# Optimization experiments

Measured on AMD Instinct MI355X. Metric: run time of the kernel, lower is better.

## Reference

```python
import jax, jax.numpy as jnp
import numpy as np

TIMESTEPS = 32
MAX_LATENCY = 1.0


def setup_inputs() -> dict:
    key = jax.random.key(0)
    data = jax.random.uniform(key, (32, 256, 256), dtype=jnp.float32)
    return {"data": data}


def reference(data):
    # data: [B, H, W] (any trailing dims). Output: [B, T, H, W].
    T = TIMESTEPS
    d_min = data.min()
    d_max = data.max()
    denom = jnp.maximum(d_max - d_min, jnp.asarray(1e-12, data.dtype))
    normalized = jnp.where(d_max > d_min, (data - d_min) / denom,
                           jnp.full_like(data, 0.5))
    latencies = (1.0 - normalized) * MAX_LATENCY
    # torch .long() truncates toward zero; latencies >= 0 so floor == trunc
    spike_times = jnp.clip((latencies * (T - 1)).astype(jnp.int32), 0, T - 1)
    # one-hot over timestep axis, then move it next to batch: [B, ..., T] -> [B, T, ...]
    spike_train = jax.nn.one_hot(spike_times, T, dtype=jnp.float32)
    return jnp.moveaxis(spike_train, -1, 1)
```

## Files before the change

kernel.cpp:

```cpp
#include <hip/hip_runtime.h>

#define TSTEPS 32
#define HW 65536
#define NB 32
#define N_ELEM (NB * HW)
#define N4 (N_ELEM / 4)
#define RED_BLOCKS 1024

__device__ __forceinline__ unsigned int f2key(float f) {
    unsigned int u = __float_as_uint(f);
    return (u & 0x80000000u) ? ~u : (u | 0x80000000u);
}
__device__ __forceinline__ float key2f(unsigned int k) {
    unsigned int u = (k & 0x80000000u) ? (k & 0x7fffffffu) : ~k;
    return __uint_as_float(u);
}

__global__ void lc_partial(const float4* __restrict__ in, unsigned int* __restrict__ ws) {
    __shared__ unsigned int smin[4], sinv[4];
    int tid = threadIdx.x;
    int i0  = blockIdx.x * 512 + tid;
    unsigned int kmin = 0xFFFFFFFFu, kinv = 0xFFFFFFFFu;
    #pragma unroll
    for (int j = 0; j < 2; ++j) {
        float4 v = in[i0 + j * 256];
        unsigned int k;
        k = f2key(v.x); kmin = min(kmin, k); kinv = min(kinv, ~k);
        k = f2key(v.y); kmin = min(kmin, k); kinv = min(kinv, ~k);
        k = f2key(v.z); kmin = min(kmin, k); kinv = min(kinv, ~k);
        k = f2key(v.w); kmin = min(kmin, k); kinv = min(kinv, ~k);
    }
    #pragma unroll
    for (int off = 32; off >= 1; off >>= 1) {
        kmin = min(kmin, (unsigned int)__shfl_xor((int)kmin, off, 64));
        kinv = min(kinv, (unsigned int)__shfl_xor((int)kinv, off, 64));
    }
    int wave = tid >> 6;
    if ((tid & 63) == 0) { smin[wave] = kmin; sinv[wave] = kinv; }
    __syncthreads();
    if (tid == 0) {
        #pragma unroll
        for (int w = 1; w < 4; ++w) {
            kmin = min(kmin, smin[w]);
            kinv = min(kinv, sinv[w]);
        }
        ws[blockIdx.x]              = kmin;
        ws[RED_BLOCKS + blockIdx.x] = kinv;
    }
}

__device__ __forceinline__ int spike_t(float x, float mn, float denom, bool valid) {
    float n   = valid ? ((x - mn) / denom) : 0.5f;
    float lat = 1.0f - n;
    int   t   = (int)(lat * 31.0f);
    t = t < 0 ? 0 : t;
    t = t > (TSTEPS - 1) ? (TSTEPS - 1) : t;
    return t;
}

__global__ void lc_spike(const float4* __restrict__ in, float* __restrict__ out,
                         const unsigned int* __restrict__ ws) {
    __shared__ unsigned int smin[4], sinv[4];
    __shared__ float s_mn, s_mx;
    int tid = threadIdx.x;

    uint4 a = reinterpret_cast<const uint4*>(ws)[tid];
    uint4 c = reinterpret_cast<const uint4*>(ws + RED_BLOCKS)[tid];
    unsigned int kmin = min(min(a.x, a.y), min(a.z, a.w));
    unsigned int kinv = min(min(c.x, c.y), min(c.z, c.w));
    #pragma unroll
    for (int off = 32; off >= 1; off >>= 1) {
        kmin = min(kmin, (unsigned int)__shfl_xor((int)kmin, off, 64));
        kinv = min(kinv, (unsigned int)__shfl_xor((int)kinv, off, 64));
    }
    int wave = tid >> 6;
    if ((tid & 63) == 0) { smin[wave] = kmin; sinv[wave] = kinv; }
    __syncthreads();
    if (tid == 0) {
        #pragma unroll
        for (int w = 1; w < 4; ++w) {
            kmin = min(kmin, smin[w]);
            kinv = min(kinv, sinv[w]);
        }
        s_mn = key2f(kmin);
        s_mx = key2f(~kinv);
    }
    __syncthreads();

    float mn = s_mn, mx = s_mx;
    bool  valid = (mx > mn);
    float denom = fmaxf(mx - mn, 1e-12f);

    int idx = blockIdx.x * blockDim.x + tid;
    int b   = idx >> 14;
    int rem = idx & 16383;

    float4 v = in[idx];
    int t0 = spike_t(v.x, mn, denom, valid);
    int t1 = spike_t(v.y, mn, denom, valid);
    int t2 = spike_t(v.z, mn, denom, valid);
    int t3 = spike_t(v.w, mn, denom, valid);

    float* base = out + (size_t)b * TSTEPS * HW + (size_t)rem * 4;
    #pragma unroll
    for (int tt = 0; tt < TSTEPS; ++tt) {
        float4 o;
        o.x = (tt == t0) ? 1.0f : 0.0f;
        o.y = (tt == t1) ? 1.0f : 0.0f;
        o.z = (tt == t2) ? 1.0f : 0.0f;
        o.w = (tt == t3) ? 1.0f : 0.0f;
        *reinterpret_cast<float4*>(base + (size_t)tt * HW) = o;
    }
}

extern "C" void kernel_launch(void* const* d_in, const int* in_sizes, int n_in,
                              void* d_out, int out_size, void* d_ws, size_t ws_size,
                              hipStream_t stream) {
    const float4*  in = (const float4*)d_in[0];
    float*        out = (float*)d_out;
    unsigned int*  ws = (unsigned int*)d_ws;

    lc_partial<<<RED_BLOCKS, 256, 0, stream>>>(in, ws);
    lc_spike<<<N4 / 256, 256, 0, stream>>>(in, out, ws);
}
```

Baseline: 47.89 us.

## Fuse min/max reduction and spike writes into one kernel via grid barrier

Merges the partial-reduction kernel and the spike-writing kernel into one persistent launch of 1024 blocks. The blocks synchronise through an atomic-counter grid barrier after publishing their partial min/max. Each thread keeps its two input float4s in registers, so the input is read once instead of twice and one kernel launch disappears. It adds a memset of the counter and relies on all 1024 blocks being co-resident, otherwise the spin-wait barrier deadlocks. It also serialises every block on the slowest one before any output is written.

```diff
diff --git a/kernel.cpp b/kernel.cpp
--- a/kernel.cpp
+++ b/kernel.cpp
@@ -5,7 +5,8 @@
 #define NB 32
 #define N_ELEM (NB * HW)
 #define N4 (N_ELEM / 4)
-#define RED_BLOCKS 1024
+#define GRID 1024
+#define CTR 2048
 
 __device__ __forceinline__ unsigned int f2key(float f) {
     unsigned int u = __float_as_uint(f);
@@ -16,20 +17,36 @@
     return __uint_as_float(u);
 }
 
-__global__ void lc_partial(const float4* __restrict__ in, unsigned int* __restrict__ ws) {
+__device__ __forceinline__ int spike_t(float x, float mn, float denom, bool valid) {
+    float n   = valid ? ((x - mn) / denom) : 0.5f;
+    float lat = 1.0f - n;
+    int   t   = (int)(lat * 31.0f);
+    t = t < 0 ? 0 : t;
+    t = t > (TSTEPS - 1) ? (TSTEPS - 1) : t;
+    return t;
+}
+
+__global__ __launch_bounds__(256, 4)
+void lc_fused(const float4* __restrict__ in, float* __restrict__ out,
+              unsigned int* __restrict__ ws) {
     __shared__ unsigned int smin[4], sinv[4];
+    __shared__ float s_mn, s_mx;
     int tid = threadIdx.x;
     int i0  = blockIdx.x * 512 + tid;
-    unsigned int kmin = 0xFFFFFFFFu, kinv = 0xFFFFFFFFu;
-    #pragma unroll
-    for (int j = 0; j < 2; ++j) {
-        float4 v = in[i0 + j * 256];
-        unsigned int k;
-        k = f2key(v.x); kmin = min(kmin, k); kinv = min(kinv, ~k);
-        k = f2key(v.y); kmin = min(kmin, k); kinv = min(kinv, ~k);
-        k = f2key(v.z); kmin = min(kmin, k); kinv = min(kinv, ~k);
-        k = f2key(v.w); kmin = min(kmin, k); kinv = min(kinv, ~k);
-    }
+    int i1  = i0 + 256;
+
+    float4 v0 = in[i0];
+    float4 v1 = in[i1];
+
+    unsigned int kmin = 0xFFFFFFFFu, kinv = 0xFFFFFFFFu, k;
+    k = f2key(v0.x); kmin = min(kmin, k); kinv = min(kinv, ~k);
+    k = f2key(v0.y); kmin = min(kmin, k); kinv = min(kinv, ~k);
+    k = f2key(v0.z); kmin = min(kmin, k); kinv = min(kinv, ~k);
+    k = f2key(v0.w); kmin = min(kmin, k); kinv = min(kinv, ~k);
+    k = f2key(v1.x); kmin = min(kmin, k); kinv = min(kinv, ~k);
+    k = f2key(v1.y); kmin = min(kmin, k); kinv = min(kinv, ~k);
+    k = f2key(v1.z); kmin = min(kmin, k); kinv = min(kinv, ~k);
+    k = f2key(v1.w); kmin = min(kmin, k); kinv = min(kinv, ~k);
     #pragma unroll
     for (int off = 32; off >= 1; off >>= 1) {
         kmin = min(kmin, (unsigned int)__shfl_xor((int)kmin, off, 64));
@@ -44,36 +61,28 @@
             kmin = min(kmin, smin[w]);
             kinv = min(kinv, sinv[w]);
         }
-        ws[blockIdx.x]              = kmin;
-        ws[RED_BLOCKS + blockIdx.x] = kinv;
+        ws[blockIdx.x]        = kmin;
+        ws[GRID + blockIdx.x] = kinv;
+        __threadfence();
+        __hip_atomic_fetch_add(&ws[CTR], 1u, __ATOMIC_ACQ_REL,
+                               __HIP_MEMORY_SCOPE_AGENT);
+        while (__hip_atomic_load(&ws[CTR], __ATOMIC_ACQUIRE,
+                                 __HIP_MEMORY_SCOPE_AGENT) < GRID) {
+            __builtin_amdgcn_s_sleep(2);
+        }
+        __threadfence();
     }
-}
-
-__device__ __forceinline__ int spike_t(float x, float mn, float denom, bool valid) {
-    float n   = valid ? ((x - mn) / denom) : 0.5f;
-    float lat = 1.0f - n;
-    int   t   = (int)(lat * 31.0f);
-    t = t < 0 ? 0 : t;
-    t = t > (TSTEPS - 1) ? (TSTEPS - 1) : t;
-    return t;
-}
-
-__global__ void lc_spike(const float4* __restrict__ in, float* __restrict__ out,
-                         const unsigned int* __restrict__ ws) {
-    __shared__ unsigned int smin[4], sinv[4];
-    __shared__ float s_mn, s_mx;
-    int tid = threadIdx.x;
+    __syncthreads();
 
     uint4 a = reinterpret_cast<const uint4*>(ws)[tid];
-    uint4 c = reinterpret_cast<const uint4*>(ws + RED_BLOCKS)[tid];
-    unsigned int kmin = min(min(a.x, a.y), min(a.z, a.w));
-    unsigned int kinv = min(min(c.x, c.y), min(c.z, c.w));
+    uint4 c = reinterpret_cast<const uint4*>(ws + GRID)[tid];
+    kmin = min(min(a.x, a.y), min(a.z, a.w));
+    kinv = min(min(c.x, c.y), min(c.z, c.w));
     #pragma unroll
     for (int off = 32; off >= 1; off >>= 1) {
         kmin = min(kmin, (unsigned int)__shfl_xor((int)kmin, off, 64));
         kinv = min(kinv, (unsigned int)__shfl_xor((int)kinv, off, 64));
     }
-    int wave = tid >> 6;
     if ((tid & 63) == 0) { smin[wave] = kmin; sinv[wave] = kinv; }
     __syncthreads();
     if (tid == 0) {
@@ -91,25 +100,34 @@
     bool  valid = (mx > mn);
     float denom = fmaxf(mx - mn, 1e-12f);
 
-    int idx = blockIdx.x * blockDim.x + tid;
-    int b   = idx >> 14;
-    int rem = idx & 16383;
+    int t00 = spike_t(v0.x, mn, denom, valid);
+    int t01 = spike_t(v0.y, mn, denom, valid);
+    int t02 = spike_t(v0.z, mn, denom, valid);
+    int t03 = spike_t(v0.w, mn, denom, valid);
+    int t10 = spike_t(v1.x, mn, denom, valid);
+    int t11 = spike_t(v1.y, mn, denom, valid);
+    int t12 = spike_t(v1.z, mn, denom, valid);
+    int t13 = spike_t(v1.w, mn, denom, valid);
 
-    float4 v = in[idx];
-    int t0 = spike_t(v.x, mn, denom, valid);
-    int t1 = spike_t(v.y, mn, denom, valid);
-    int t2 = spike_t(v.z, mn, denom, valid);
-    int t3 = spike_t(v.w, mn, denom, valid);
+    int b    = i0 >> 14;
+    int rem0 = i0 & 16383;
+    int rem1 = i1 & 16383;
+    float* base0 = out + (size_t)b * TSTEPS * HW + (size_t)rem0 * 4;
+    float* base1 = out + (size_t)b * TSTEPS * HW + (size_t)rem1 * 4;
 
-    float* base = out + (size_t)b * TSTEPS * HW + (size_t)rem * 4;
     #pragma unroll
     for (int tt = 0; tt < TSTEPS; ++tt) {
-        float4 o;
-        o.x = (tt == t0) ? 1.0f : 0.0f;
-        o.y = (tt == t1) ? 1.0f : 0.0f;
-        o.z = (tt == t2) ? 1.0f : 0.0f;
-        o.w = (tt == t3) ? 1.0f : 0.0f;
-        *reinterpret_cast<float4*>(base + (size_t)tt * HW) = o;
+        float4 o0, o1;
+        o0.x = (tt == t00) ? 1.0f : 0.0f;
+        o0.y = (tt == t01) ? 1.0f : 0.0f;
+        o0.z = (tt == t02) ? 1.0f : 0.0f;
+        o0.w = (tt == t03) ? 1.0f : 0.0f;
+        o1.x = (tt == t10) ? 1.0f : 0.0f;
+        o1.y = (tt == t11) ? 1.0f : 0.0f;
+        o1.z = (tt == t12) ? 1.0f : 0.0f;
+        o1.w = (tt == t13) ? 1.0f : 0.0f;
+        *reinterpret_cast<float4*>(base0 + (size_t)tt * HW) = o0;
+        *reinterpret_cast<float4*>(base1 + (size_t)tt * HW) = o1;
     }
 }
 
@@ -120,6 +138,6 @@
     float*        out = (float*)d_out;
     unsigned int*  ws = (unsigned int*)d_ws;
 
-    lc_partial<<<RED_BLOCKS, 256, 0, stream>>>(in, ws);
-    lc_spike<<<N4 / 256, 256, 0, stream>>>(in, out, ws);
+    (void)hipMemsetAsync(ws + CTR, 0, sizeof(unsigned int), stream);
+    lc_fused<<<GRID, 256, 0, stream>>>(in, out, ws);
 }
```

Measured after the change: 108.4 us. 126% more time.

## Split spike kernel into packed timestep map and plane-wise gather writer

Applied to the files above, without the earlier changes.

Adds a kernel that computes each element's spike timestep once and stores four of them packed as bytes into workspace. A second kernel then writes each output timestep plane contiguously, reading the small packed map. The aim is to replace the old pattern of strided writes across 32 planes per thread with fully contiguous streaming stores. The cost is an extra launch and extra workspace traffic. The old path remains as a fallback when the workspace is too small.

```diff
diff --git a/kernel.cpp b/kernel.cpp
--- a/kernel.cpp
+++ b/kernel.cpp
@@ -2,10 +2,13 @@
 
 #define TSTEPS 32
 #define HW 65536
+#define HW4 16384
 #define NB 32
 #define N_ELEM (NB * HW)
 #define N4 (N_ELEM / 4)
 #define RED_BLOCKS 1024
+#define TOFF 2048
+#define WS_NEEDED ((TOFF + N4) * sizeof(unsigned int))
 
 __device__ __forceinline__ unsigned int f2key(float f) {
     unsigned int u = __float_as_uint(f);
@@ -58,12 +61,11 @@
     return t;
 }
 
-__global__ void lc_spike(const float4* __restrict__ in, float* __restrict__ out,
-                         const unsigned int* __restrict__ ws) {
+__device__ __forceinline__ void reduce_partials(const unsigned int* __restrict__ ws,
+                                                float& mn, float& mx) {
     __shared__ unsigned int smin[4], sinv[4];
     __shared__ float s_mn, s_mx;
     int tid = threadIdx.x;
-
     uint4 a = reinterpret_cast<const uint4*>(ws)[tid];
     uint4 c = reinterpret_cast<const uint4*>(ws + RED_BLOCKS)[tid];
     unsigned int kmin = min(min(a.x, a.y), min(a.z, a.w));
@@ -86,12 +88,60 @@
         s_mx = key2f(~kinv);
     }
     __syncthreads();
+    mn = s_mn; mx = s_mx;
+}
 
-    float mn = s_mn, mx = s_mx;
+__global__ void lc_tmap(const float4* __restrict__ in, unsigned int* __restrict__ ws) {
+    float mn, mx;
+    reduce_partials(ws, mn, mx);
     bool  valid = (mx > mn);
     float denom = fmaxf(mx - mn, 1e-12f);
 
-    int idx = blockIdx.x * blockDim.x + tid;
+    int tid = threadIdx.x;
+    int i0  = blockIdx.x * 512 + tid;
+    unsigned int* tmap = ws + TOFF;
+    #pragma unroll
+    for (int j = 0; j < 2; ++j) {
+        int i = i0 + j * 256;
+        float4 v = in[i];
+        unsigned int p =  (unsigned int)spike_t(v.x, mn, denom, valid)
+                       | ((unsigned int)spike_t(v.y, mn, denom, valid) << 8)
+                       | ((unsigned int)spike_t(v.z, mn, denom, valid) << 16)
+                       | ((unsigned int)spike_t(v.w, mn, denom, valid) << 24);
+        tmap[i] = p;
+    }
+}
+
+__global__ void lc_gather(const unsigned int* __restrict__ ws, float4* __restrict__ out) {
+    const unsigned int* tmap = ws + TOFF;
+    int blk   = blockIdx.x;
+    int plane = blk >> 4;
+    unsigned int tt = (unsigned int)(plane & 31);
+    int b     = plane >> 5;
+    int base4 = (blk & 15) * 1024 + threadIdx.x;
+    const unsigned int* tp = tmap + b * HW4;
+    float4* op = out + (size_t)plane * HW4;
+    #pragma unroll
+    for (int j = 0; j < 4; ++j) {
+        int h = base4 + j * 256;
+        unsigned int tw = tp[h];
+        float4 o;
+        o.x = (( tw        & 255u) == tt) ? 1.0f : 0.0f;
+        o.y = (((tw >> 8)  & 255u) == tt) ? 1.0f : 0.0f;
+        o.z = (((tw >> 16) & 255u) == tt) ? 1.0f : 0.0f;
+        o.w = (( tw >> 24        ) == tt) ? 1.0f : 0.0f;
+        op[h] = o;
+    }
+}
+
+__global__ void lc_spike(const float4* __restrict__ in, float* __restrict__ out,
+                         const unsigned int* __restrict__ ws) {
+    float mn, mx;
+    reduce_partials(ws, mn, mx);
+    bool  valid = (mx > mn);
+    float denom = fmaxf(mx - mn, 1e-12f);
+
+    int idx = blockIdx.x * blockDim.x + threadIdx.x;
     int b   = idx >> 14;
     int rem = idx & 16383;
 
@@ -117,9 +167,13 @@
                               void* d_out, int out_size, void* d_ws, size_t ws_size,
                               hipStream_t stream) {
     const float4*  in = (const float4*)d_in[0];
-    float*        out = (float*)d_out;
     unsigned int*  ws = (unsigned int*)d_ws;
 
     lc_partial<<<RED_BLOCKS, 256, 0, stream>>>(in, ws);
-    lc_spike<<<N4 / 256, 256, 0, stream>>>(in, out, ws);
+    if (ws_size >= WS_NEEDED) {
+        lc_tmap<<<RED_BLOCKS, 256, 0, stream>>>(in, ws);
+        lc_gather<<<NB * TSTEPS * 16, 256, 0, stream>>>(ws, (float4*)d_out);
+    } else {
+        lc_spike<<<N4 / 256, 256, 0, stream>>>(in, (float*)d_out, ws);
+    }
 }
```

Result: slower. 49.78 us (+4.0%).
